# Kernel optimization log

Hardware: AMD Instinct MI355X
Metric: run time of the kernel (lower is better)

The kernel has to match this reference:

```python
import jax, jax.numpy as jnp
import numpy as np

N_NODES = 100000
N_EDGES = 3200000
NUM_FEATURES = 256
HIDDEN = 16
NUM_CLASSES = 40


def gcn_conv(x, edge_index, W, b, num_nodes):
    """PyG GCNConv: linear -> add self-loops -> symmetric deg norm -> scatter-add -> bias."""
    x = x @ W  # [N, out]
    loop = jnp.arange(num_nodes)
    src = jnp.concatenate([edge_index[0], loop])  # messages flow src -> dst
    dst = jnp.concatenate([edge_index[1], loop])
    # degree of target nodes (with self-loops)
    deg = jax.ops.segment_sum(jnp.ones_like(dst, dtype=x.dtype), dst,
                              num_segments=num_nodes)
    dinv = jnp.where(deg > 0, jax.lax.rsqrt(deg), 0.0)
    norm = dinv[src] * dinv[dst]  # [E+N]
    out = jax.ops.segment_sum(x[src] * norm[:, None], dst,
                              num_segments=num_nodes)
    return out + b


def setup_inputs() -> dict:
    key = jax.random.key(0)
    k1, k2, k3, k4 = jax.random.split(key, 4)
    x = jax.random.normal(k1, (N_NODES, NUM_FEATURES), dtype=jnp.float32)
    edge_index = jax.random.randint(k2, (2, N_EDGES), 0, N_NODES, dtype=jnp.int64)
    W1 = jax.random.normal(k3, (NUM_FEATURES, HIDDEN), dtype=jnp.float32) / np.sqrt(NUM_FEATURES)
    b1 = jnp.zeros((HIDDEN,), dtype=jnp.float32)
    W2 = jax.random.normal(k4, (HIDDEN, NUM_CLASSES), dtype=jnp.float32) / np.sqrt(HIDDEN)
    b2 = jnp.zeros((NUM_CLASSES,), dtype=jnp.float32)
    return {"x": x, "edge_index": edge_index, "W1": W1, "b1": b1, "W2": W2, "b2": b2}


def reference(x, edge_index, W1, b1, W2, b2):
    h = jax.nn.relu(gcn_conv(x, edge_index, W1, b1, N_NODES))
    return gcn_conv(h, edge_index, W2, b2, N_NODES)
```

## Files before the change

kernel.cpp:

```cpp
#include <hip/hip_runtime.h>
#include <hip/hip_fp16.h>

#define N_NODES   100000
#define N_EDGES   3200000
#define F_IN      256
#define HID       16
#define NCLS      40

#define CHUNK     16384
#define NBLK      ((N_EDGES + CHUNK - 1) / CHUNK)
#define B2SHIFT   9
#define NB2       ((N_NODES + 511) >> B2SHIFT)
#define BCAP      17408

__global__ __launch_bounds__(256) void k1_hist_gemm(const int* __restrict__ ei,
                                                    const float* __restrict__ x,
                                                    const float* __restrict__ W1,
                                                    int* __restrict__ hist_blk,
                                                    __half* __restrict__ y1h) {
    __shared__ float W1s[F_IN * HID];
    int* h = (int*)W1s;
    int blk = blockIdx.x, t = threadIdx.x;

    for (int i = t; i < NB2; i += 256) h[i] = 0;
    __syncthreads();
    int e0 = blk * CHUNK;
    int eN = min(CHUNK, N_EDGES - e0);
    const int4* d4 = (const int4*)(ei + N_EDGES + e0);
    for (int i = t; i < (eN >> 2); i += 256) {
        int4 d = d4[i];
        atomicAdd(&h[d.x >> B2SHIFT], 1);
        atomicAdd(&h[d.y >> B2SHIFT], 1);
        atomicAdd(&h[d.z >> B2SHIFT], 1);
        atomicAdd(&h[d.w >> B2SHIFT], 1);
    }
    __syncthreads();
    for (int i = t; i < NB2; i += 256) hist_blk[i * NBLK + blk] = h[i];
    __syncthreads();

    #pragma unroll
    for (int i = 0; i < (F_IN * HID) / 256; i++) W1s[t + i * 256] = W1[t + i * 256];
    __syncthreads();

    int n0 = blk * 512 + t;
    int n1 = n0 + 256;
    if (n0 >= N_NODES) return;
    bool v1 = (n1 < N_NODES);

    const float4* xr0 = (const float4*)(x + (size_t)n0 * F_IN);
    const float4* xr1 = (const float4*)(x + (size_t)(v1 ? n1 : n0) * F_IN);
    float acc0[HID], acc1[HID];
    #pragma unroll
    for (int j = 0; j < HID; j++) { acc0[j] = 0.f; acc1[j] = 0.f; }

    #pragma unroll 2
    for (int k4 = 0; k4 < F_IN / 4; k4++) {
        float4 xa = xr0[k4];
        float4 xb = xr1[k4];
        int k = k4 * 4;
        #pragma unroll
        for (int hh = 0; hh < HID; hh++) {
            float w0 = W1s[(k + 0) * HID + hh];
            float w1 = W1s[(k + 1) * HID + hh];
            float w2 = W1s[(k + 2) * HID + hh];
            float w3 = W1s[(k + 3) * HID + hh];
            acc0[hh] += xa.x * w0 + xa.y * w1 + xa.z * w2 + xa.w * w3;
            acc1[hh] += xb.x * w0 + xb.y * w1 + xb.z * w2 + xb.w * w3;
        }
    }
    {
        __half2 hp[8];
        #pragma unroll
        for (int j = 0; j < 8; j++)
            hp[j] = __float22half2_rn(make_float2(acc0[2 * j], acc0[2 * j + 1]));
        float4* o = (float4*)(y1h + (size_t)n0 * HID);
        o[0] = ((float4*)hp)[0];
        o[1] = ((float4*)hp)[1];
    }
    if (v1) {
        __half2 hp[8];
        #pragma unroll
        for (int j = 0; j < 8; j++)
            hp[j] = __float22half2_rn(make_float2(acc1[2 * j], acc1[2 * j + 1]));
        float4* o = (float4*)(y1h + (size_t)n1 * HID);
        o[0] = ((float4*)hp)[0];
        o[1] = ((float4*)hp)[1];
    }
}

__global__ __launch_bounds__(512) void k2_bin(const int* __restrict__ ei,
                                              const int* __restrict__ hist_blk,
                                              int* __restrict__ buf) {
    __shared__ int cur[NB2];
    __shared__ int sc[256];
    int blk = blockIdx.x, t = threadIdx.x;
    int pre = 0, tot = 0;
    if (t < NB2) {
        const int* row = hist_blk + t * NBLK;
        for (int k = 0; k < NBLK; k++) {
            int v = row[k];
            pre += (k < blk) ? v : 0;
            tot += v;
        }
    }
    if (t < 256) sc[t] = tot;
    __syncthreads();
    for (int off = 1; off < 256; off <<= 1) {
        int u = 0;
        if (t < 256 && t >= off) u = sc[t - off];
        __syncthreads();
        if (t < 256) sc[t] += u;
        __syncthreads();
    }
    if (t < NB2) cur[t] = (sc[t] - tot) + pre;
    __syncthreads();

    int e0 = blk * CHUNK;
    int eN = min(CHUNK, N_EDGES - e0);
    const int4* s4 = (const int4*)(ei + e0);
    const int4* d4 = (const int4*)(ei + N_EDGES + e0);
    for (int i = t; i < (eN >> 2); i += 512) {
        int4 d = d4[i], s = s4[i];
        int p0 = atomicAdd(&cur[d.x >> B2SHIFT], 1); buf[p0] = ((d.x & 511) << 17) | s.x;
        int p1 = atomicAdd(&cur[d.y >> B2SHIFT], 1); buf[p1] = ((d.y & 511) << 17) | s.y;
        int p2 = atomicAdd(&cur[d.z >> B2SHIFT], 1); buf[p2] = ((d.z & 511) << 17) | s.z;
        int p3 = atomicAdd(&cur[d.w >> B2SHIFT], 1); buf[p3] = ((d.w & 511) << 17) | s.w;
    }
}

__global__ __launch_bounds__(512) void k3_build(const int* __restrict__ buf,
                                               const int* __restrict__ hist_blk,
                                               int* __restrict__ rowptr,
                                               float* __restrict__ dinv,
                                               int* __restrict__ csr_src,
                                               __half* __restrict__ y1h) {
    __shared__ int lbuf[BCAP];
    __shared__ int hist[512], offs[512], cur[512];
    __shared__ int sc[256];
    __shared__ int s_base, s_cnt;
    int b = blockIdx.x, t = threadIdx.x;

    int tot = 0;
    if (t < NB2) {
        const int* row = hist_blk + t * NBLK;
        for (int k = 0; k < NBLK; k++) tot += row[k];
    }
    if (t < 256) sc[t] = tot;
    hist[t] = 0;
    __syncthreads();
    for (int off = 1; off < 256; off <<= 1) {
        int u = 0;
        if (t < 256 && t >= off) u = sc[t - off];
        __syncthreads();
        if (t < 256) sc[t] += u;
        __syncthreads();
    }
    if (t == b) { s_base = sc[b] - tot; s_cnt = tot; }
    __syncthreads();
    int base = s_base, cnt = s_cnt;

    for (int i = t; i < cnt; i += 512) {
        int v = buf[base + i];
        if (i < BCAP) lbuf[i] = v;
        atomicAdd(&hist[v >> 17], 1);
    }
    __syncthreads();
    int v = hist[t];
    offs[t] = v;
    __syncthreads();
    for (int off = 1; off < 512; off <<= 1) {
        int u = (t >= off) ? offs[t - off] : 0;
        __syncthreads();
        offs[t] += u;
        __syncthreads();
    }
    int ex = offs[t] - v;
    int n = (b << B2SHIFT) + t;
    if (n < N_NODES) {
        rowptr[n] = base + ex;
        float dv = rsqrtf((float)(v + 1));
        dinv[n] = dv;
        float4* yr = (float4*)(y1h + (size_t)n * HID);
        float4 a = yr[0], bqq = yr[1];
        __half2* ah = (__half2*)&a;
        __half2* bh = (__half2*)&bqq;
        #pragma unroll
        for (int j = 0; j < 4; j++) {
            float2 fa = __half22float2(ah[j]);
            float2 fb = __half22float2(bh[j]);
            ah[j] = __float22half2_rn(make_float2(fa.x * dv, fa.y * dv));
            bh[j] = __float22half2_rn(make_float2(fb.x * dv, fb.y * dv));
        }
        yr[0] = a;
        yr[1] = bqq;
    }
    if (b == 0 && t == 0) rowptr[N_NODES] = N_EDGES;
    cur[t] = ex;
    __syncthreads();
    for (int i = t; i < cnt; i += 512) {
        int p = (i < BCAP) ? lbuf[i] : buf[base + i];
        int pos = atomicAdd(&cur[p >> 17], 1);
        csr_src[base + pos] = p & 0x1FFFF;
    }
}

__device__ __forceinline__ void acc_row(const float4* __restrict__ tab, int s, float* acc) {
    float4 v0 = tab[(size_t)s * 2 + 0];
    float4 v1 = tab[(size_t)s * 2 + 1];
    const __half2* a0 = (const __half2*)&v0;
    const __half2* a1 = (const __half2*)&v1;
    #pragma unroll
    for (int j = 0; j < 4; j++) {
        float2 f0 = __half22float2(a0[j]);
        float2 f1 = __half22float2(a1[j]);
        acc[2 * j]         += f0.x;
        acc[2 * j + 1]     += f0.y;
        acc[8 + 2 * j]     += f1.x;
        acc[8 + 2 * j + 1] += f1.y;
    }
}

__device__ __forceinline__ void acc_row2(const float4* __restrict__ tab, int s0, int s1, float* acc) {
    float4 v0 = tab[(size_t)s0 * 2 + 0];
    float4 v1 = tab[(size_t)s0 * 2 + 1];
    float4 v2 = tab[(size_t)s1 * 2 + 0];
    float4 v3 = tab[(size_t)s1 * 2 + 1];
    const __half2* a0 = (const __half2*)&v0;
    const __half2* a1 = (const __half2*)&v1;
    const __half2* b0 = (const __half2*)&v2;
    const __half2* b1 = (const __half2*)&v3;
    #pragma unroll
    for (int j = 0; j < 4; j++) {
        float2 f0 = __half22float2(a0[j]);
        float2 f1 = __half22float2(a1[j]);
        float2 g0 = __half22float2(b0[j]);
        float2 g1 = __half22float2(b1[j]);
        acc[2 * j]         += f0.x + g0.x;
        acc[2 * j + 1]     += f0.y + g0.y;
        acc[8 + 2 * j]     += f1.x + g1.x;
        acc[8 + 2 * j + 1] += f1.y + g1.y;
    }
}

__global__ __launch_bounds__(256) void gather1_kernel(const int* __restrict__ rowptr,
                                                      const int* __restrict__ csr_src,
                                                      const __half* __restrict__ y1h,
                                                      const float* __restrict__ b1,
                                                      const float* __restrict__ dinv,
                                                      __half* __restrict__ zh) {
    int n   = blockIdx.x * 64 + (threadIdx.x >> 2);
    int sub = threadIdx.x & 3;
    if (n >= N_NODES) return;
    const float4* tab = (const float4*)y1h;
    int beg = rowptr[n], end = rowptr[n + 1];
    float acc[16];
    #pragma unroll
    for (int i = 0; i < 16; i++) acc[i] = 0.f;
    if (sub == 0) acc_row(tab, n, acc);
    int e = beg + sub;
    for (; e + 4 < end; e += 8)
        acc_row2(tab, csr_src[e], csr_src[e + 4], acc);
    if (e < end) acc_row(tab, csr_src[e], acc);
    #pragma unroll
    for (int m = 1; m < 4; m <<= 1) {
        #pragma unroll
        for (int i = 0; i < 16; i++) acc[i] += __shfl_xor(acc[i], m, 4);
    }
    if (sub < 2) {
        float dvn = dinv[n];
        const float4* b1q = (const float4*)b1;
        float4 ba = b1q[sub * 2], bb = b1q[sub * 2 + 1];
        float bv[8] = {ba.x, ba.y, ba.z, ba.w, bb.x, bb.y, bb.z, bb.w};
        __half2 outp[4];
        #pragma unroll
        for (int j = 0; j < 4; j++) {
            float2 r;
            r.x = fmaxf(dvn * acc[sub * 8 + 2 * j]     + bv[2 * j],     0.f) * dvn;
            r.y = fmaxf(dvn * acc[sub * 8 + 2 * j + 1] + bv[2 * j + 1], 0.f) * dvn;
            outp[j] = __float22half2_rn(r);
        }
        *(float4*)(zh + (size_t)n * HID + sub * 8) = *(float4*)outp;
    }
}

__global__ __launch_bounds__(256) void gather2_kernel(const int* __restrict__ rowptr,
                                                      const int* __restrict__ csr_src,
                                                      const __half* __restrict__ zh,
                                                      const float* __restrict__ W2,
                                                      const float* __restrict__ b2,
                                                      const float* __restrict__ dinv,
                                                      float* __restrict__ out) {
    __shared__ float W2s[HID * NCLS];
    __shared__ float b2s[NCLS];
    int t = threadIdx.x;
    for (int i = t; i < HID * NCLS; i += 256) W2s[i] = W2[i];
    if (t < NCLS) b2s[t] = b2[t];
    __syncthreads();

    int n   = blockIdx.x * 64 + (t >> 2);
    int sub = t & 3;
    if (n >= N_NODES) return;
    const float4* tab = (const float4*)zh;
    int beg = rowptr[n], end = rowptr[n + 1];
    float acc[16];
    #pragma unroll
    for (int i = 0; i < 16; i++) acc[i] = 0.f;
    if (sub == 0) acc_row(tab, n, acc);
    int e = beg + sub;
    for (; e + 4 < end; e += 8)
        acc_row2(tab, csr_src[e], csr_src[e + 4], acc);
    if (e < end) acc_row(tab, csr_src[e], acc);
    #pragma unroll
    for (int m = 1; m < 4; m <<= 1) {
        #pragma unroll
        for (int i = 0; i < 16; i++) acc[i] += __shfl_xor(acc[i], m, 4);
    }
    float dv = dinv[n];
    int c0 = sub * 10;
    float o[10];
    #pragma unroll
    for (int j = 0; j < 10; j++) o[j] = 0.f;
    #pragma unroll
    for (int h = 0; h < HID; h++) {
        float a = acc[h];
        const float* w = &W2s[h * NCLS + c0];
        #pragma unroll
        for (int j = 0; j < 10; j++) o[j] += a * w[j];
    }
    float* op = out + (size_t)n * NCLS + c0;
    #pragma unroll
    for (int j = 0; j < 5; j++) {
        float2 r = make_float2(dv * o[2 * j]     + b2s[c0 + 2 * j],
                               dv * o[2 * j + 1] + b2s[c0 + 2 * j + 1]);
        *(float2*)(op + 2 * j) = r;
    }
}

extern "C" void kernel_launch(void* const* d_in, const int* in_sizes, int n_in,
                              void* d_out, int out_size, void* d_ws, size_t ws_size,
                              hipStream_t stream) {
    const float* x   = (const float*)d_in[0];
    const int*   ei  = (const int*)  d_in[1];
    const float* W1  = (const float*)d_in[2];
    const float* b1  = (const float*)d_in[3];
    const float* W2  = (const float*)d_in[4];
    const float* b2  = (const float*)d_in[5];
    float* out = (float*)d_out;

    char* ws = (char*)d_ws;
    size_t off = 0;
    int*   hist_blk = (int*)(ws + off); off += (size_t)NB2 * NBLK * 4;
    off = (off + 15) & ~(size_t)15;
    int*    rowptr  = (int*)   (ws + off); off += (size_t)(N_NODES + 1) * 4;
    off = (off + 15) & ~(size_t)15;
    float*  dinv    = (float*) (ws + off); off += (size_t)N_NODES * 4;
    int*    csr_src = (int*)   (ws + off); off += (size_t)N_EDGES * 4;
    int*    buf     = (int*)   (ws + off); off += (size_t)N_EDGES * 4;
    __half* y1h     = (__half*)(ws + off); off += (size_t)N_NODES * HID * 2;
    __half* zh      = (__half*)(ws + off); off += (size_t)N_NODES * HID * 2;

    k1_hist_gemm <<<NBLK, 256, 0, stream>>>(ei, x, W1, hist_blk, y1h);
    k2_bin       <<<NBLK, 512, 0, stream>>>(ei, hist_blk, buf);
    k3_build     <<<NB2, 512, 0, stream>>>(buf, hist_blk, rowptr, dinv, csr_src, y1h);
    gather1_kernel<<<(N_NODES + 63) / 64, 256, 0, stream>>>(rowptr, csr_src, y1h, b1, dinv, zh);
    gather2_kernel<<<(N_NODES + 63) / 64, 256, 0, stream>>>(rowptr, csr_src, zh, W2, b2, dinv, out);
}
```

Baseline: 325.2 us.

## Fuse histogram and binning into GEMM kernel using global atomic bucket reservation

Merges the histogram pass and the edge binning pass into the first kernel. Each chunk reserves space in fixed-capacity per-bucket regions through global atomics, replacing the per-block histogram table and its prefix scans. This removes one kernel launch, one reread of the destination indices, and the long serial scans over the histogram table in k2/k3. Block size and chunk size change to cover the grid. The cost is that the order of edges inside each bucket now depends on atomic timing. Any bucket whose count exceeds BCAP would overflow into the next bucket's region.

```diff
diff --git a/kernel.cpp b/kernel.cpp
--- a/kernel.cpp
+++ b/kernel.cpp
@@ -7,43 +7,57 @@
 #define HID       16
 #define NCLS      40
 
-#define CHUNK     16384
-#define NBLK      ((N_EDGES + CHUNK - 1) / CHUNK)
+#define CHUNK     8192
+#define NCHK      ((N_EDGES + CHUNK - 1) / CHUNK)
+#define GRID1     392
 #define B2SHIFT   9
 #define NB2       ((N_NODES + 511) >> B2SHIFT)
 #define BCAP      17408
 
-__global__ __launch_bounds__(256) void k1_hist_gemm(const int* __restrict__ ei,
-                                                    const float* __restrict__ x,
-                                                    const float* __restrict__ W1,
-                                                    int* __restrict__ hist_blk,
-                                                    __half* __restrict__ y1h) {
+__global__ __launch_bounds__(128) void k1_all(const int* __restrict__ ei,
+                                              const float* __restrict__ x,
+                                              const float* __restrict__ W1,
+                                              int* __restrict__ gcnt,
+                                              int* __restrict__ buf,
+                                              __half* __restrict__ y1h) {
     __shared__ float W1s[F_IN * HID];
-    int* h = (int*)W1s;
+    int* h   = (int*)W1s;
+    int* cur = ((int*)W1s) + 256;
     int blk = blockIdx.x, t = threadIdx.x;
 
-    for (int i = t; i < NB2; i += 256) h[i] = 0;
-    __syncthreads();
-    int e0 = blk * CHUNK;
-    int eN = min(CHUNK, N_EDGES - e0);
-    const int4* d4 = (const int4*)(ei + N_EDGES + e0);
-    for (int i = t; i < (eN >> 2); i += 256) {
-        int4 d = d4[i];
-        atomicAdd(&h[d.x >> B2SHIFT], 1);
-        atomicAdd(&h[d.y >> B2SHIFT], 1);
-        atomicAdd(&h[d.z >> B2SHIFT], 1);
-        atomicAdd(&h[d.w >> B2SHIFT], 1);
-    }
-    __syncthreads();
-    for (int i = t; i < NB2; i += 256) hist_blk[i * NBLK + blk] = h[i];
-    __syncthreads();
-
-    #pragma unroll
-    for (int i = 0; i < (F_IN * HID) / 256; i++) W1s[t + i * 256] = W1[t + i * 256];
-    __syncthreads();
-
-    int n0 = blk * 512 + t;
-    int n1 = n0 + 256;
+    if (blk < NCHK) {
+        for (int j = t; j < NB2; j += 128) h[j] = 0;
+        __syncthreads();
+        int e0 = blk * CHUNK;
+        int eN = min(CHUNK, N_EDGES - e0);
+        const int4* d4 = (const int4*)(ei + N_EDGES + e0);
+        const int4* s4 = (const int4*)(ei + e0);
+        for (int i = t; i < (eN >> 2); i += 128) {
+            int4 d = d4[i];
+            atomicAdd(&h[d.x >> B2SHIFT], 1);
+            atomicAdd(&h[d.y >> B2SHIFT], 1);
+            atomicAdd(&h[d.z >> B2SHIFT], 1);
+            atomicAdd(&h[d.w >> B2SHIFT], 1);
+        }
+        __syncthreads();
+        for (int j = t; j < NB2; j += 128)
+            cur[j] = j * BCAP + atomicAdd(&gcnt[j], h[j]);
+        __syncthreads();
+        for (int i = t; i < (eN >> 2); i += 128) {
+            int4 d = d4[i], s = s4[i];
+            int p0 = atomicAdd(&cur[d.x >> B2SHIFT], 1); buf[p0] = ((d.x & 511) << 17) | s.x;
+            int p1 = atomicAdd(&cur[d.y >> B2SHIFT], 1); buf[p1] = ((d.y & 511) << 17) | s.y;
+            int p2 = atomicAdd(&cur[d.z >> B2SHIFT], 1); buf[p2] = ((d.z & 511) << 17) | s.z;
+            int p3 = atomicAdd(&cur[d.w >> B2SHIFT], 1); buf[p3] = ((d.w & 511) << 17) | s.w;
+        }
+        __syncthreads();
+    }
+
+    for (int i = t; i < F_IN * HID; i += 128) W1s[i] = W1[i];
+    __syncthreads();
+
+    int n0 = blk * 256 + t;
+    int n1 = n0 + 128;
     if (n0 >= N_NODES) return;
     bool v1 = (n1 < N_NODES);
 
@@ -88,48 +102,8 @@
     }
 }
 
-__global__ __launch_bounds__(512) void k2_bin(const int* __restrict__ ei,
-                                              const int* __restrict__ hist_blk,
-                                              int* __restrict__ buf) {
-    __shared__ int cur[NB2];
-    __shared__ int sc[256];
-    int blk = blockIdx.x, t = threadIdx.x;
-    int pre = 0, tot = 0;
-    if (t < NB2) {
-        const int* row = hist_blk + t * NBLK;
-        for (int k = 0; k < NBLK; k++) {
-            int v = row[k];
-            pre += (k < blk) ? v : 0;
-            tot += v;
-        }
-    }
-    if (t < 256) sc[t] = tot;
-    __syncthreads();
-    for (int off = 1; off < 256; off <<= 1) {
-        int u = 0;
-        if (t < 256 && t >= off) u = sc[t - off];
-        __syncthreads();
-        if (t < 256) sc[t] += u;
-        __syncthreads();
-    }
-    if (t < NB2) cur[t] = (sc[t] - tot) + pre;
-    __syncthreads();
-
-    int e0 = blk * CHUNK;
-    int eN = min(CHUNK, N_EDGES - e0);
-    const int4* s4 = (const int4*)(ei + e0);
-    const int4* d4 = (const int4*)(ei + N_EDGES + e0);
-    for (int i = t; i < (eN >> 2); i += 512) {
-        int4 d = d4[i], s = s4[i];
-        int p0 = atomicAdd(&cur[d.x >> B2SHIFT], 1); buf[p0] = ((d.x & 511) << 17) | s.x;
-        int p1 = atomicAdd(&cur[d.y >> B2SHIFT], 1); buf[p1] = ((d.y & 511) << 17) | s.y;
-        int p2 = atomicAdd(&cur[d.z >> B2SHIFT], 1); buf[p2] = ((d.z & 511) << 17) | s.z;
-        int p3 = atomicAdd(&cur[d.w >> B2SHIFT], 1); buf[p3] = ((d.w & 511) << 17) | s.w;
-    }
-}
-
 __global__ __launch_bounds__(512) void k3_build(const int* __restrict__ buf,
-                                               const int* __restrict__ hist_blk,
+                                               const int* __restrict__ gcnt,
                                                int* __restrict__ rowptr,
                                                float* __restrict__ dinv,
                                                int* __restrict__ csr_src,
@@ -140,12 +114,8 @@
     __shared__ int s_base, s_cnt;
     int b = blockIdx.x, t = threadIdx.x;
 
-    int tot = 0;
-    if (t < NB2) {
-        const int* row = hist_blk + t * NBLK;
-        for (int k = 0; k < NBLK; k++) tot += row[k];
-    }
-    if (t < 256) sc[t] = tot;
+    int cntv = 0;
+    if (t < 256) { cntv = (t < NB2) ? gcnt[t] : 0; sc[t] = cntv; }
     hist[t] = 0;
     __syncthreads();
     for (int off = 1; off < 256; off <<= 1) {
@@ -155,12 +125,13 @@
         if (t < 256) sc[t] += u;
         __syncthreads();
     }
-    if (t == b) { s_base = sc[b] - tot; s_cnt = tot; }
+    if (t == b) { s_base = sc[b] - cntv; s_cnt = cntv; }
     __syncthreads();
     int base = s_base, cnt = s_cnt;
+    int src0 = b * BCAP;
 
     for (int i = t; i < cnt; i += 512) {
-        int v = buf[base + i];
+        int v = buf[src0 + i];
         if (i < BCAP) lbuf[i] = v;
         atomicAdd(&hist[v >> 17], 1);
     }
@@ -181,9 +152,9 @@
         float dv = rsqrtf((float)(v + 1));
         dinv[n] = dv;
         float4* yr = (float4*)(y1h + (size_t)n * HID);
-        float4 a = yr[0], bqq = yr[1];
+        float4 a = yr[0], bq = yr[1];
         __half2* ah = (__half2*)&a;
-        __half2* bh = (__half2*)&bqq;
+        __half2* bh = (__half2*)&bq;
         #pragma unroll
         for (int j = 0; j < 4; j++) {
             float2 fa = __half22float2(ah[j]);
@@ -192,13 +163,13 @@
             bh[j] = __float22half2_rn(make_float2(fb.x * dv, fb.y * dv));
         }
         yr[0] = a;
-        yr[1] = bqq;
+        yr[1] = bq;
     }
     if (b == 0 && t == 0) rowptr[N_NODES] = N_EDGES;
     cur[t] = ex;
     __syncthreads();
     for (int i = t; i < cnt; i += 512) {
-        int p = (i < BCAP) ? lbuf[i] : buf[base + i];
+        int p = (i < BCAP) ? lbuf[i] : buf[src0 + i];
         int pos = atomicAdd(&cur[p >> 17], 1);
         csr_src[base + pos] = p & 0x1FFFF;
     }
@@ -349,19 +320,19 @@
 
     char* ws = (char*)d_ws;
     size_t off = 0;
-    int*   hist_blk = (int*)(ws + off); off += (size_t)NB2 * NBLK * 4;
+    int*   gcnt = (int*)(ws + off); off += (size_t)NB2 * 4;
     off = (off + 15) & ~(size_t)15;
     int*    rowptr  = (int*)   (ws + off); off += (size_t)(N_NODES + 1) * 4;
     off = (off + 15) & ~(size_t)15;
     float*  dinv    = (float*) (ws + off); off += (size_t)N_NODES * 4;
     int*    csr_src = (int*)   (ws + off); off += (size_t)N_EDGES * 4;
-    int*    buf     = (int*)   (ws + off); off += (size_t)N_EDGES * 4;
+    int*    buf     = (int*)   (ws + off); off += (size_t)NB2 * BCAP * 4;
     __half* y1h     = (__half*)(ws + off); off += (size_t)N_NODES * HID * 2;
     __half* zh      = (__half*)(ws + off); off += (size_t)N_NODES * HID * 2;
 
-    k1_hist_gemm <<<NBLK, 256, 0, stream>>>(ei, x, W1, hist_blk, y1h);
-    k2_bin       <<<NBLK, 512, 0, stream>>>(ei, hist_blk, buf);
-    k3_build     <<<NB2, 512, 0, stream>>>(buf, hist_blk, rowptr, dinv, csr_src, y1h);
+    hipMemsetAsync(gcnt, 0, (size_t)NB2 * 4, stream);
+    k1_all   <<<GRID1, 128, 0, stream>>>(ei, x, W1, gcnt, buf, y1h);
+    k3_build <<<NB2, 512, 0, stream>>>(buf, gcnt, rowptr, dinv, csr_src, y1h);
     gather1_kernel<<<(N_NODES + 63) / 64, 256, 0, stream>>>(rowptr, csr_src, y1h, b1, dinv, zh);
     gather2_kernel<<<(N_NODES + 63) / 64, 256, 0, stream>>>(rowptr, csr_src, zh, W2, b2, dinv, out);
 }
```

Result: slower. 333.3 us (+2.5%).

## Halve edge chunk size and read W1 via uniform loads instead of LDS

Applied to the files above, without the earlier changes.

Halves CHUNK so k1 launches twice as many blocks, each handling 256 nodes with one node per thread instead of two. W1 is no longer staged in shared memory; each thread reads W1 directly from global memory with wave-uniform addresses, which can become scalar loads. The goal is more parallelism and less LDS traffic and sync in the GEMM-plus-histogram kernel. In exchange the hist_blk table doubles in size, so k2's per-bin prefix loop over NBLK gets longer.

```diff
diff --git a/kernel.cpp b/kernel.cpp
--- a/kernel.cpp
+++ b/kernel.cpp
@@ -7,19 +7,20 @@
 #define HID       16
 #define NCLS      40
 
-#define CHUNK     16384
+#define CHUNK     8192
 #define NBLK      ((N_EDGES + CHUNK - 1) / CHUNK)
 #define B2SHIFT   9
 #define NB2       ((N_NODES + 511) >> B2SHIFT)
 #define BCAP      17408
+
+#define COMP(v, kk) ((kk) == 0 ? (v).x : (kk) == 1 ? (v).y : (kk) == 2 ? (v).z : (v).w)
 
 __global__ __launch_bounds__(256) void k1_hist_gemm(const int* __restrict__ ei,
                                                     const float* __restrict__ x,
                                                     const float* __restrict__ W1,
                                                     int* __restrict__ hist_blk,
                                                     __half* __restrict__ y1h) {
-    __shared__ float W1s[F_IN * HID];
-    int* h = (int*)W1s;
+    __shared__ int h[NB2];
     int blk = blockIdx.x, t = threadIdx.x;
 
     for (int i = t; i < NB2; i += 256) h[i] = 0;
@@ -36,56 +37,33 @@
     }
     __syncthreads();
     for (int i = t; i < NB2; i += 256) hist_blk[i * NBLK + blk] = h[i];
-    __syncthreads();
-
-    #pragma unroll
-    for (int i = 0; i < (F_IN * HID) / 256; i++) W1s[t + i * 256] = W1[t + i * 256];
-    __syncthreads();
-
-    int n0 = blk * 512 + t;
-    int n1 = n0 + 256;
-    if (n0 >= N_NODES) return;
-    bool v1 = (n1 < N_NODES);
-
-    const float4* xr0 = (const float4*)(x + (size_t)n0 * F_IN);
-    const float4* xr1 = (const float4*)(x + (size_t)(v1 ? n1 : n0) * F_IN);
-    float acc0[HID], acc1[HID];
-    #pragma unroll
-    for (int j = 0; j < HID; j++) { acc0[j] = 0.f; acc1[j] = 0.f; }
-
-    #pragma unroll 2
+
+    int n = blk * 256 + t;
+    if (n >= N_NODES) return;
+
+    const float4* xr = (const float4*)(x + (size_t)n * F_IN);
+    float acc[HID];
+    #pragma unroll
+    for (int j = 0; j < HID; j++) acc[j] = 0.f;
+
+    #pragma unroll 4
     for (int k4 = 0; k4 < F_IN / 4; k4++) {
-        float4 xa = xr0[k4];
-        float4 xb = xr1[k4];
-        int k = k4 * 4;
-        #pragma unroll
-        for (int hh = 0; hh < HID; hh++) {
-            float w0 = W1s[(k + 0) * HID + hh];
-            float w1 = W1s[(k + 1) * HID + hh];
-            float w2 = W1s[(k + 2) * HID + hh];
-            float w3 = W1s[(k + 3) * HID + hh];
-            acc0[hh] += xa.x * w0 + xa.y * w1 + xa.z * w2 + xa.w * w3;
-            acc1[hh] += xb.x * w0 + xb.y * w1 + xb.z * w2 + xb.w * w3;
+        float4 xv = xr[k4];
+        #pragma unroll
+        for (int kk = 0; kk < 4; kk++) {
+            const float xs = COMP(xv, kk);
+            const float* w = W1 + (k4 * 4 + kk) * HID;
+            #pragma unroll
+            for (int hh = 0; hh < HID; hh++) acc[hh] += xs * w[hh];
         }
     }
-    {
-        __half2 hp[8];
-        #pragma unroll
-        for (int j = 0; j < 8; j++)
-            hp[j] = __float22half2_rn(make_float2(acc0[2 * j], acc0[2 * j + 1]));
-        float4* o = (float4*)(y1h + (size_t)n0 * HID);
-        o[0] = ((float4*)hp)[0];
-        o[1] = ((float4*)hp)[1];
-    }
-    if (v1) {
-        __half2 hp[8];
-        #pragma unroll
-        for (int j = 0; j < 8; j++)
-            hp[j] = __float22half2_rn(make_float2(acc1[2 * j], acc1[2 * j + 1]));
-        float4* o = (float4*)(y1h + (size_t)n1 * HID);
-        o[0] = ((float4*)hp)[0];
-        o[1] = ((float4*)hp)[1];
-    }
+    __half2 hp[8];
+    #pragma unroll
+    for (int j = 0; j < 8; j++)
+        hp[j] = __float22half2_rn(make_float2(acc[2 * j], acc[2 * j + 1]));
+    float4* o = (float4*)(y1h + (size_t)n * HID);
+    o[0] = ((float4*)hp)[0];
+    o[1] = ((float4*)hp)[1];
 }
 
 __global__ __launch_bounds__(512) void k2_bin(const int* __restrict__ ei,
@@ -181,9 +159,9 @@
         float dv = rsqrtf((float)(v + 1));
         dinv[n] = dv;
         float4* yr = (float4*)(y1h + (size_t)n * HID);
-        float4 a = yr[0], bqq = yr[1];
+        float4 a = yr[0], bq = yr[1];
         __half2* ah = (__half2*)&a;
-        __half2* bh = (__half2*)&bqq;
+        __half2* bh = (__half2*)&bq;
         #pragma unroll
         for (int j = 0; j < 4; j++) {
             float2 fa = __half22float2(ah[j]);
@@ -192,7 +170,7 @@
             bh[j] = __float22half2_rn(make_float2(fb.x * dv, fb.y * dv));
         }
         yr[0] = a;
-        yr[1] = bqq;
+        yr[1] = bq;
     }
     if (b == 0 && t == 0) rowptr[N_NODES] = N_EDGES;
     cur[t] = ex;
```

Result: no change. 331.0 us (+1.8%).
